# Performance work log

Hardware: AMD Instinct MI355X
Metric: run time of the kernel (lower is better)

Reference implementation:

```python
import jax, jax.numpy as jnp
import numpy as np

D = 512
B, S = 4, 4096


def setup_inputs() -> dict:
    key = jax.random.key(0)
    ks = jax.random.split(key, 8)
    scale = 1.0 / np.sqrt(D)
    return {
        "x": jax.random.normal(ks[0], (B, S, D), dtype=jnp.float32),
        "bias": jax.random.normal(ks[1], (1, S, S), dtype=jnp.float32),
        "Wq_w": jax.random.normal(ks[2], (D, D), dtype=jnp.float32) * scale,
        "Wq_b": jax.random.normal(ks[3], (D,), dtype=jnp.float32) * 0.02,
        "Wk_w": jax.random.normal(ks[4], (D, D), dtype=jnp.float32) * scale,
        "Wk_b": jax.random.normal(ks[5], (D,), dtype=jnp.float32) * 0.02,
        "Wv_w": jax.random.normal(ks[6], (D, D), dtype=jnp.float32) * scale,
        "Wv_b": jax.random.normal(ks[7], (D,), dtype=jnp.float32) * 0.02,
    }


def reference(x, bias, Wq_w, Wq_b, Wk_w, Wk_b, Wv_w, Wv_b):
    # torch nn.Linear: y = x @ W.T + b
    q = jnp.einsum("bsd,ed->bse", x, Wq_w) + Wq_b
    k = jnp.einsum("bsd,ed->bse", x, Wk_w) + Wk_b
    v = jnp.einsum("bsd,ed->bse", x, Wv_w) + Wv_b
    inv_sqrt_d = jnp.asarray(1.0 / np.sqrt(D), dtype=x.dtype)
    # scores: [B, S, S] -- scale by sqrt(feature_dim) as in the original
    scores = jnp.einsum("bqd,bkd->bqk", q * inv_sqrt_d, k) + bias
    weights = jax.nn.sigmoid(scores)
    out = jnp.einsum("bqk,bkd->bqd", weights, v)
    return out
```

## Files before the change

kernel.cpp:

```cpp
#include <hip/hip_runtime.h>
#include <hip/hip_bf16.h>
#include <stdint.h>

typedef unsigned short bf16_t;
typedef __attribute__((ext_vector_type(4))) short s4v;
typedef __attribute__((ext_vector_type(8))) short short8;
typedef __attribute__((ext_vector_type(4))) float f32x4;

__device__ __forceinline__ bf16_t f2b(float f) {
    union { float f; uint32_t u; } v; v.f = f;
    uint32_t u = v.u;
    return (bf16_t)((u + 0x7FFFu + ((u >> 16) & 1u)) >> 16);
}

__global__ __launch_bounds__(256) void cvt_f32_bf16(const float* __restrict__ in,
                                                    bf16_t* __restrict__ out, int n4) {
    int i = blockIdx.x * blockDim.x + threadIdx.x;
    if (i >= n4) return;
    float4 f = ((const float4*)in)[i];
    ushort4 o;
    o.x = f2b(f.x); o.y = f2b(f.y); o.z = f2b(f.z); o.w = f2b(f.w);
    ((ushort4*)out)[i] = o;
}

__global__ __launch_bounds__(256) void cvt_w3(const float* __restrict__ a,
                                              const float* __restrict__ b,
                                              const float* __restrict__ c,
                                              bf16_t* __restrict__ out) {
    int i = blockIdx.x * blockDim.x + threadIdx.x;
    const int which = i >> 16;
    const int idx   = i & 65535;
    const float* src = (which == 0) ? a : (which == 1) ? b : c;
    float4 f = ((const float4*)src)[idx];
    ushort4 o;
    o.x = f2b(f.x); o.y = f2b(f.y); o.z = f2b(f.z); o.w = f2b(f.w);
    ((ushort4*)out)[i] = o;
}

__device__ __forceinline__ void lds_dma16(const void* g, void* l) {
    __builtin_amdgcn_global_load_lds(
        (const __attribute__((address_space(1))) void*)g,
        (__attribute__((address_space(3))) void*)l, 16, 0, 0);
}


__global__ __launch_bounds__(256)
void proj_all(const bf16_t* __restrict__ Xb, const bf16_t* __restrict__ Wb,
              const float* __restrict__ qb, const float* __restrict__ kb,
              const float* __restrict__ vb,
              bf16_t* __restrict__ Qb, bf16_t* __restrict__ Kb,
              bf16_t* __restrict__ Vt)
{
    __shared__ __align__(16) bf16_t lds[16384];
    bf16_t* lsA = lds;
    bf16_t* lsB = lds + 8192;

    const int tid  = threadIdx.x;
    const int lane = tid & 63;
    const int w    = tid >> 6;
    const int wm   = w & 1, wn = w >> 1;
    const int ll   = lane & 15;
    const int quad = lane >> 4;

    const int bid   = blockIdx.x;
    const int x     = bid & 7;
    const int g     = bid >> 3;
    const int mi    = x * 16 + g / 12;
    const int inner = g % 12;
    const int m0 = mi * 128;
    const int n0 = (inner & 3) * 128;
    const int z  = inner >> 2;

    const bf16_t* A = Xb;
    const bf16_t* B = Wb + z * 262144;

    f32x4 acc[4][4];
#pragma unroll
    for (int i = 0; i < 4; i++)
#pragma unroll
        for (int j = 0; j < 4; j++) acc[i][j] = (f32x4){0.f, 0.f, 0.f, 0.f};

    for (int k0 = 0; k0 < 512; k0 += 64) {
#pragma unroll
        for (int c = 0; c < 4; ++c) {
            const int base = (c * 4 + w) * 64;
            const int slot = base + lane;
            const int row  = slot >> 3;
            const int kc   = ((slot & 7) ^ (row & 7)) << 3;
            lds_dma16(A + (size_t)(m0 + row) * 512 + k0 + kc, (char*)lsA + base * 16);
            lds_dma16(B + (size_t)(n0 + row) * 512 + k0 + kc, (char*)lsB + base * 16);
        }
        __syncthreads();

#pragma unroll
        for (int t = 0; t < 2; t++) {
            short8 af[4], bf[4];
#pragma unroll
            for (int i = 0; i < 4; i++) {
                const int ri = wm * 64 + i * 16 + ll;
                const int rj = wn * 64 + i * 16 + ll;
                af[i] = *(const short8*)(lsA + ri * 64 + (((t * 4 + quad) ^ (ll & 7)) << 3));
                bf[i] = *(const short8*)(lsB + rj * 64 + (((t * 4 + quad) ^ (ll & 7)) << 3));
            }
#pragma unroll
            for (int i = 0; i < 4; i++)
#pragma unroll
                for (int j = 0; j < 4; j++)
                    acc[i][j] = __builtin_amdgcn_mfma_f32_16x16x32_bf16(af[i], bf[j], acc[i][j], 0, 0, 0);
        }
        __syncthreads();
    }

    bf16_t* wbuf = lds + w * 4096;
    const float inv = 0.044194173824159216f;

    if (z != 2) {
        const float* bptr = (z == 0) ? qb : kb;
        const float scl   = (z == 0) ? inv : 1.0f;
#pragma unroll
        for (int j = 0; j < 4; j++) {
            const int colL = j * 16 + ll;
            const float bv = bptr[n0 + wn * 64 + colL];
#pragma unroll
            for (int i = 0; i < 4; i++) {
                f32x4 a = acc[i][j];
#pragma unroll
                for (int r = 0; r < 4; r++) {
                    const int rowL = i * 16 + quad * 4 + r;
                    wbuf[rowL * 64 + (colL ^ ((rowL & 7) << 3))] = f2b((a[r] + bv) * scl);
                }
            }
        }
        __syncthreads();
        bf16_t* dst = (z == 0) ? Qb : Kb;
        const int rowg0 = m0 + wm * 64;
        const int colg0 = n0 + wn * 64;
#pragma unroll
        for (int k = 0; k < 8; k++) {
            const int rowL = (lane >> 3) + k * 8;
            const int c0   = (lane & 7) * 8;
            short8 vv = *(const short8*)(wbuf + rowL * 64 + (c0 ^ ((rowL & 7) << 3)));
            *(short8*)(dst + (size_t)(rowg0 + rowL) * 512 + colg0 + c0) = vv;
        }
    } else {
#pragma unroll
        for (int j = 0; j < 4; j++) {
            const int d = j * 16 + ll;
            const float bv = vb[n0 + wn * 64 + d];
#pragma unroll
            for (int i = 0; i < 4; i++) {
                f32x4 a = acc[i][j];
                s4v pk;
                pk[0] = (short)f2b(a[0] + bv);
                pk[1] = (short)f2b(a[1] + bv);
                pk[2] = (short)f2b(a[2] + bv);
                pk[3] = (short)f2b(a[3] + bv);
                const int sB = i * 16 + quad * 4;
                *(s4v*)(wbuf + d * 64 + (sB ^ ((d & 7) << 3))) = pk;
            }
        }
        __syncthreads();
        const int rowg0 = m0 + wm * 64;
        const int b  = rowg0 >> 12;
        const int s0 = rowg0 & 4095;
        const int d0 = n0 + wn * 64;
#pragma unroll
        for (int k = 0; k < 8; k++) {
            const int dL = (lane >> 3) + k * 8;
            const int c0 = (lane & 7) * 8;
            short8 vv = *(const short8*)(wbuf + dL * 64 + (c0 ^ ((dL & 7) << 3)));
            *(short8*)(Vt + ((size_t)b * 512 + d0 + dL) * 4096 + s0 + c0) = vv;
        }
    }
}

__global__ __launch_bounds__(256)
void scores_sig(const bf16_t* __restrict__ Qb, const bf16_t* __restrict__ Kb,
                const float* __restrict__ bias, bf16_t* __restrict__ P)
{
    __shared__ bf16_t lsA[128 * 64];
    __shared__ bf16_t lsB[128 * 64];

    const int tid  = threadIdx.x;
    const int lane = tid & 63;
    const int w    = tid >> 6;
    const int wm   = w & 1, wn = w >> 1;
    const int ll   = lane & 15;
    const int quad = lane >> 4;

    const int bx  = blockIdx.x;
    const int z   = bx & 3;
    const int t_  = bx >> 2;
    const int sup = t_ >> 5;
    const int win = t_ & 31;
    const int m0  = ((sup >> 2) * 4 + (win & 3)) * 128;
    const int n0  = ((sup & 3) * 8 + (win >> 2)) * 128;

    const bf16_t* A = Qb + (size_t)z * 2097152;
    const bf16_t* B = Kb + (size_t)z * 2097152;
    bf16_t* out = P + (size_t)z * 16777216;

    f32x4 acc[4][4];
#pragma unroll
    for (int i = 0; i < 4; i++)
#pragma unroll
        for (int j = 0; j < 4; j++) acc[i][j] = (f32x4){0.f, 0.f, 0.f, 0.f};

    for (int k0 = 0; k0 < 512; k0 += 64) {
#pragma unroll
        for (int c = 0; c < 4; ++c) {
            const int base = (c * 4 + w) * 64;
            const int slot = base + lane;
            const int row  = slot >> 3;
            const int kc   = ((slot & 7) ^ (row & 7)) << 3;
            lds_dma16(A + (size_t)(m0 + row) * 512 + k0 + kc, (char*)lsA + base * 16);
            lds_dma16(B + (size_t)(n0 + row) * 512 + k0 + kc, (char*)lsB + base * 16);
        }
        __syncthreads();

#pragma unroll
        for (int t = 0; t < 2; t++) {
            short8 af[4], bf[4];
#pragma unroll
            for (int i = 0; i < 4; i++) {
                const int ri = wm * 64 + i * 16 + ll;
                const int rj = wn * 64 + i * 16 + ll;
                af[i] = *(const short8*)(lsA + ri * 64 + (((t * 4 + quad) ^ (ll & 7)) << 3));
                bf[i] = *(const short8*)(lsB + rj * 64 + (((t * 4 + quad) ^ (ll & 7)) << 3));
            }
#pragma unroll
            for (int i = 0; i < 4; i++)
#pragma unroll
                for (int j = 0; j < 4; j++)
                    acc[i][j] = __builtin_amdgcn_mfma_f32_16x16x32_bf16(af[i], bf[j], acc[i][j], 0, 0, 0);
        }
        __syncthreads();
    }

#pragma unroll
    for (int i = 0; i < 4; i++) {
#pragma unroll
        for (int j = 0; j < 4; j++) {
            const int col  = n0 + wn * 64 + j * 16 + ll;
            const int rowb = m0 + wm * 64 + i * 16 + quad * 4;
            f32x4 a = acc[i][j];
#pragma unroll
            for (int r = 0; r < 4; r++) {
                const int row = rowb + r;
                const float v = a[r] + bias[(size_t)row * 4096 + col];
                const float p = __builtin_amdgcn_rcpf(1.f + __expf(-v));
                out[(size_t)row * 4096 + col] = (bf16_t)(__float_as_uint(p) >> 16);
            }
        }
    }
}

__global__ __launch_bounds__(256)
void pv_gemm(const bf16_t* __restrict__ P, const bf16_t* __restrict__ Vt,
             float* __restrict__ outg)
{
    __shared__ __align__(16) bf16_t lsA[128 * 64];
    __shared__ __align__(16) bf16_t lsB[128 * 64];

    const int tid  = threadIdx.x;
    const int lane = tid & 63;
    const int w    = tid >> 6;
    const int wm   = w & 1, wn = w >> 1;
    const int ll   = lane & 15;
    const int quad = lane >> 4;

    const int n0 = blockIdx.x * 128;
    const int m0 = blockIdx.y * 128;
    const int z  = blockIdx.z;

    const bf16_t* A = P + (size_t)z * 16777216;
    const bf16_t* B = Vt + (size_t)z * 2097152;
    float* out = outg + (size_t)z * 2097152;

    f32x4 acc[4][4];
#pragma unroll
    for (int i = 0; i < 4; i++)
#pragma unroll
        for (int j = 0; j < 4; j++) acc[i][j] = (f32x4){0.f, 0.f, 0.f, 0.f};

    for (int k0 = 0; k0 < 4096; k0 += 64) {
#pragma unroll
        for (int c = 0; c < 4; ++c) {
            const int base = (c * 4 + w) * 64;
            const int slot = base + lane;
            const int row  = slot >> 3;
            const int kc   = ((slot & 7) ^ (row & 7)) << 3;
            lds_dma16(A + (size_t)(m0 + row) * 4096 + k0 + kc, (char*)lsA + base * 16);
            lds_dma16(B + (size_t)(n0 + row) * 4096 + k0 + kc, (char*)lsB + base * 16);
        }
        __syncthreads();

#pragma unroll
        for (int t = 0; t < 2; t++) {
            short8 af[4], bf[4];
#pragma unroll
            for (int i = 0; i < 4; i++) {
                const int ri = wm * 64 + i * 16 + ll;
                const int rj = wn * 64 + i * 16 + ll;
                af[i] = *(const short8*)(lsA + ri * 64 + (((t * 4 + quad) ^ (ll & 7)) << 3));
                bf[i] = *(const short8*)(lsB + rj * 64 + (((t * 4 + quad) ^ (ll & 7)) << 3));
            }
#pragma unroll
            for (int i = 0; i < 4; i++)
#pragma unroll
                for (int j = 0; j < 4; j++)
                    acc[i][j] = __builtin_amdgcn_mfma_f32_16x16x32_bf16(af[i], bf[j], acc[i][j], 0, 0, 0);
        }
        __syncthreads();
    }

#pragma unroll
    for (int i = 0; i < 4; i++) {
#pragma unroll
        for (int j = 0; j < 4; j++) {
            const int col  = n0 + wn * 64 + j * 16 + ll;
            const int rowb = m0 + wm * 64 + i * 16 + quad * 4;
            f32x4 a = acc[i][j];
#pragma unroll
            for (int r = 0; r < 4; r++)
                out[(size_t)(rowb + r) * 512 + col] = a[r];
        }
    }
}

extern "C" void kernel_launch(void* const* d_in, const int* in_sizes, int n_in,
                              void* d_out, int out_size, void* d_ws, size_t ws_size,
                              hipStream_t stream) {
    (void)in_sizes; (void)n_in; (void)out_size; (void)ws_size;
    const float* x    = (const float*)d_in[0];
    const float* bias = (const float*)d_in[1];
    const float* Wq_w = (const float*)d_in[2];
    const float* Wq_b = (const float*)d_in[3];
    const float* Wk_w = (const float*)d_in[4];
    const float* Wk_b = (const float*)d_in[5];
    const float* Wv_w = (const float*)d_in[6];
    const float* Wv_b = (const float*)d_in[7];
    float* out = (float*)d_out;

    bf16_t* Xb = (bf16_t*)d_ws;
    bf16_t* Wb = Xb + (size_t)16384 * 512;
    bf16_t* Qb = Wb + (size_t)3 * 512 * 512;
    bf16_t* Kb = Qb + (size_t)16384 * 512;
    bf16_t* Vt = Kb + (size_t)16384 * 512;
    bf16_t* P  = Vt + (size_t)16384 * 512;

    cvt_f32_bf16<<<8192, 256, 0, stream>>>(x, Xb, 2097152);
    cvt_w3<<<768, 256, 0, stream>>>(Wq_w, Wk_w, Wv_w, Wb);

    proj_all<<<1536, 256, 0, stream>>>(Xb, Wb, Wq_b, Wk_b, Wv_b, Qb, Kb, Vt);
    scores_sig<<<4096, 256, 0, stream>>>(Qb, Kb, bias, P);
    pv_gemm<<<dim3(4, 32, 4), 256, 0, stream>>>(P, Vt, out);
}
```

Baseline: 412.6 us.

## Double-buffer LDS tiles in projection, scores and PV GEMM kernels

Each of the three GEMM kernels now uses two LDS tile buffers and issues the global-to-LDS DMA for the next K tile before computing on the current one. This drops the barrier that sat between load and compute in every K step, so memory latency can overlap with MFMA work. The cost is double the LDS per block (64 KB instead of 32 KB), which lowers how many blocks can be resident per CU. The end-of-iteration barrier still waits on all outstanding loads, so how much overlap is actually achieved depends on that wait.

```diff
diff --git a/kernel.cpp b/kernel.cpp
--- a/kernel.cpp
+++ b/kernel.cpp
@@ -51,9 +51,7 @@
               bf16_t* __restrict__ Qb, bf16_t* __restrict__ Kb,
               bf16_t* __restrict__ Vt)
 {
-    __shared__ __align__(16) bf16_t lds[16384];
-    bf16_t* lsA = lds;
-    bf16_t* lsB = lds + 8192;
+    __shared__ __align__(16) bf16_t lds[2][16384];
 
     const int tid  = threadIdx.x;
     const int lane = tid & 63;
@@ -74,24 +72,31 @@
     const bf16_t* A = Xb;
     const bf16_t* B = Wb + z * 262144;
 
-    f32x4 acc[4][4];
-#pragma unroll
-    for (int i = 0; i < 4; i++)
-#pragma unroll
-        for (int j = 0; j < 4; j++) acc[i][j] = (f32x4){0.f, 0.f, 0.f, 0.f};
-
-    for (int k0 = 0; k0 < 512; k0 += 64) {
+    auto stage = [&](int kt, int b) {
 #pragma unroll
         for (int c = 0; c < 4; ++c) {
             const int base = (c * 4 + w) * 64;
             const int slot = base + lane;
             const int row  = slot >> 3;
             const int kc   = ((slot & 7) ^ (row & 7)) << 3;
-            lds_dma16(A + (size_t)(m0 + row) * 512 + k0 + kc, (char*)lsA + base * 16);
-            lds_dma16(B + (size_t)(n0 + row) * 512 + k0 + kc, (char*)lsB + base * 16);
-        }
-        __syncthreads();
-
+            lds_dma16(A + (size_t)(m0 + row) * 512 + kt * 64 + kc, (char*)&lds[b][0]    + base * 16);
+            lds_dma16(B + (size_t)(n0 + row) * 512 + kt * 64 + kc, (char*)&lds[b][8192] + base * 16);
+        }
+    };
+
+    f32x4 acc[4][4];
+#pragma unroll
+    for (int i = 0; i < 4; i++)
+#pragma unroll
+        for (int j = 0; j < 4; j++) acc[i][j] = (f32x4){0.f, 0.f, 0.f, 0.f};
+
+    stage(0, 0);
+    __syncthreads();
+    int cur = 0;
+    for (int kt = 0; kt < 8; ++kt) {
+        if (kt < 7) stage(kt + 1, cur ^ 1);
+        const bf16_t* lsA = &lds[cur][0];
+        const bf16_t* lsB = &lds[cur][8192];
 #pragma unroll
         for (int t = 0; t < 2; t++) {
             short8 af[4], bf[4];
@@ -109,9 +114,10 @@
                     acc[i][j] = __builtin_amdgcn_mfma_f32_16x16x32_bf16(af[i], bf[j], acc[i][j], 0, 0, 0);
         }
         __syncthreads();
-    }
-
-    bf16_t* wbuf = lds + w * 4096;
+        cur ^= 1;
+    }
+
+    bf16_t* wbuf = &lds[0][0] + w * 4096;
     const float inv = 0.044194173824159216f;
 
     if (z != 2) {
@@ -178,8 +184,7 @@
 void scores_sig(const bf16_t* __restrict__ Qb, const bf16_t* __restrict__ Kb,
                 const float* __restrict__ bias, bf16_t* __restrict__ P)
 {
-    __shared__ bf16_t lsA[128 * 64];
-    __shared__ bf16_t lsB[128 * 64];
+    __shared__ __align__(16) bf16_t lds[2][16384];
 
     const int tid  = threadIdx.x;
     const int lane = tid & 63;
@@ -200,24 +205,31 @@
     const bf16_t* B = Kb + (size_t)z * 2097152;
     bf16_t* out = P + (size_t)z * 16777216;
 
-    f32x4 acc[4][4];
-#pragma unroll
-    for (int i = 0; i < 4; i++)
-#pragma unroll
-        for (int j = 0; j < 4; j++) acc[i][j] = (f32x4){0.f, 0.f, 0.f, 0.f};
-
-    for (int k0 = 0; k0 < 512; k0 += 64) {
+    auto stage = [&](int kt, int b) {
 #pragma unroll
         for (int c = 0; c < 4; ++c) {
             const int base = (c * 4 + w) * 64;
             const int slot = base + lane;
             const int row  = slot >> 3;
             const int kc   = ((slot & 7) ^ (row & 7)) << 3;
-            lds_dma16(A + (size_t)(m0 + row) * 512 + k0 + kc, (char*)lsA + base * 16);
-            lds_dma16(B + (size_t)(n0 + row) * 512 + k0 + kc, (char*)lsB + base * 16);
-        }
-        __syncthreads();
-
+            lds_dma16(A + (size_t)(m0 + row) * 512 + kt * 64 + kc, (char*)&lds[b][0]    + base * 16);
+            lds_dma16(B + (size_t)(n0 + row) * 512 + kt * 64 + kc, (char*)&lds[b][8192] + base * 16);
+        }
+    };
+
+    f32x4 acc[4][4];
+#pragma unroll
+    for (int i = 0; i < 4; i++)
+#pragma unroll
+        for (int j = 0; j < 4; j++) acc[i][j] = (f32x4){0.f, 0.f, 0.f, 0.f};
+
+    stage(0, 0);
+    __syncthreads();
+    int cur = 0;
+    for (int kt = 0; kt < 8; ++kt) {
+        if (kt < 7) stage(kt + 1, cur ^ 1);
+        const bf16_t* lsA = &lds[cur][0];
+        const bf16_t* lsB = &lds[cur][8192];
 #pragma unroll
         for (int t = 0; t < 2; t++) {
             short8 af[4], bf[4];
@@ -235,6 +247,7 @@
                     acc[i][j] = __builtin_amdgcn_mfma_f32_16x16x32_bf16(af[i], bf[j], acc[i][j], 0, 0, 0);
         }
         __syncthreads();
+        cur ^= 1;
     }
 
 #pragma unroll
@@ -259,8 +272,7 @@
 void pv_gemm(const bf16_t* __restrict__ P, const bf16_t* __restrict__ Vt,
              float* __restrict__ outg)
 {
-    __shared__ __align__(16) bf16_t lsA[128 * 64];
-    __shared__ __align__(16) bf16_t lsB[128 * 64];
+    __shared__ __align__(16) bf16_t lds[2][16384];
 
     const int tid  = threadIdx.x;
     const int lane = tid & 63;
@@ -277,24 +289,31 @@
     const bf16_t* B = Vt + (size_t)z * 2097152;
     float* out = outg + (size_t)z * 2097152;
 
-    f32x4 acc[4][4];
-#pragma unroll
-    for (int i = 0; i < 4; i++)
-#pragma unroll
-        for (int j = 0; j < 4; j++) acc[i][j] = (f32x4){0.f, 0.f, 0.f, 0.f};
-
-    for (int k0 = 0; k0 < 4096; k0 += 64) {
+    auto stage = [&](int kt, int b) {
 #pragma unroll
         for (int c = 0; c < 4; ++c) {
             const int base = (c * 4 + w) * 64;
             const int slot = base + lane;
             const int row  = slot >> 3;
             const int kc   = ((slot & 7) ^ (row & 7)) << 3;
-            lds_dma16(A + (size_t)(m0 + row) * 4096 + k0 + kc, (char*)lsA + base * 16);
-            lds_dma16(B + (size_t)(n0 + row) * 4096 + k0 + kc, (char*)lsB + base * 16);
-        }
-        __syncthreads();
-
+            lds_dma16(A + (size_t)(m0 + row) * 4096 + kt * 64 + kc, (char*)&lds[b][0]    + base * 16);
+            lds_dma16(B + (size_t)(n0 + row) * 4096 + kt * 64 + kc, (char*)&lds[b][8192] + base * 16);
+        }
+    };
+
+    f32x4 acc[4][4];
+#pragma unroll
+    for (int i = 0; i < 4; i++)
+#pragma unroll
+        for (int j = 0; j < 4; j++) acc[i][j] = (f32x4){0.f, 0.f, 0.f, 0.f};
+
+    stage(0, 0);
+    __syncthreads();
+    int cur = 0;
+    for (int kt = 0; kt < 64; ++kt) {
+        if (kt < 63) stage(kt + 1, cur ^ 1);
+        const bf16_t* lsA = &lds[cur][0];
+        const bf16_t* lsB = &lds[cur][8192];
 #pragma unroll
         for (int t = 0; t < 2; t++) {
             short8 af[4], bf[4];
@@ -312,6 +331,7 @@
                     acc[i][j] = __builtin_amdgcn_mfma_f32_16x16x32_bf16(af[i], bf[j], acc[i][j], 0, 0, 0);
         }
         __syncthreads();
+        cur ^= 1;
     }
 
 #pragma unroll
```

New measurement: 386.5 us. 1.07x faster.
